# Kernel optimization log

Hardware: AMD Instinct MI355X
Metric: run time of the kernel (lower is better)

The kernel has to match this reference:

```python
import jax, jax.numpy as jnp
import numpy as np

SEQ = 4096
EMB = 2048
DQ = 2048
DV = 2048

def setup_inputs() -> dict:
    key = jax.random.key(0)
    k1, k2, k3, k4 = jax.random.split(key, 4)
    scale = 1.0 / np.sqrt(EMB)
    return {
        "embedding_word": jax.random.normal(k1, (SEQ, EMB), dtype=jnp.float32),
        "w_q": jax.random.normal(k2, (DQ, EMB), dtype=jnp.float32) * scale,
        "w_k": jax.random.normal(k3, (DQ, EMB), dtype=jnp.float32) * scale,
        "w_v": jax.random.normal(k4, (DV, EMB), dtype=jnp.float32) * scale,
    }

def reference(embedding_word, w_q, w_k, w_v):
    # nn.Linear: y = x @ W.T (bias=False)
    q = embedding_word @ w_q.T            # [S, d_q]
    k = embedding_word @ w_k.T            # [S, d_q]
    v = embedding_word @ w_v.T            # [S, d_v]
    scores = q @ k.T                      # [S, S]
    S = scores.shape[0]
    causal = jnp.tril(jnp.ones((S, S), dtype=bool))  # True = keep
    masked = jnp.where(causal, scores, -jnp.inf)
    weights = jax.nn.softmax(masked / jnp.sqrt(jnp.float32(DQ)), axis=-1)
    return weights @ v                    # [S, d_v]
```

## Files before the change

kernel.cpp:

```cpp
#include <hip/hip_runtime.h>


using u16 = unsigned short;
typedef __bf16 bf16x8 __attribute__((ext_vector_type(8)));
typedef float  f32x4  __attribute__((ext_vector_type(4)));
typedef u16    u16x8  __attribute__((ext_vector_type(8)));

__device__ __forceinline__ u16 f2b(float f) {
  union { float f; unsigned u; } x; x.f = f;
  unsigned r = x.u + 0x7fffu + ((x.u >> 16) & 1u);
  return (u16)(r >> 16);
}
__device__ __forceinline__ float b2f(u16 h) {
  union { unsigned u; float f; } x; x.u = ((unsigned)h) << 16;
  return x.f;
}

#define GLL16(src, dst)                                                        \
  __builtin_amdgcn_global_load_lds(                                            \
      (const __attribute__((address_space(1))) void*)(src),                    \
      (__attribute__((address_space(3))) void*)(dst), 16, 0, 0)

#define MFMA_BF16(a, b, c) __builtin_amdgcn_mfma_f32_16x16x32_bf16(a, b, c, 0, 0, 0)

__global__ __launch_bounds__(256)
void cast_all(const float* __restrict__ x, const float* __restrict__ wq,
              const float* __restrict__ wk, const float* __restrict__ wv,
              u16* __restrict__ dst) {
  const int b = blockIdx.x;
  const float* src;
  size_t off;
  if (b < 4096)      { src = x;  off = (size_t)b * 2048; }
  else if (b < 6144) { src = wq; off = (size_t)(b - 4096) * 2048; }
  else if (b < 8192) { src = wk; off = (size_t)(b - 6144) * 2048; }
  else               { src = wv; off = (size_t)(b - 8192) * 2048; }
  const size_t e = off + (size_t)threadIdx.x * 8;
  float4 a = *(const float4*)(src + e);
  float4 c = *(const float4*)(src + e + 4);
  u16x8 o;
  o[0] = f2b(a.x); o[1] = f2b(a.y); o[2] = f2b(a.z); o[3] = f2b(a.w);
  o[4] = f2b(c.x); o[5] = f2b(c.y); o[6] = f2b(c.z); o[7] = f2b(c.w);
  *(u16x8*)(dst + (size_t)b * 2048 + (size_t)threadIdx.x * 8) = o;
}

__global__ __launch_bounds__(512)
void gemm_qk256(const u16* __restrict__ A, const u16* __restrict__ W,
                u16* __restrict__ Qo, u16* __restrict__ Ko) {
  extern __shared__ char lds[];
  constexpr int NT = 32;
  const int bn = blockIdx.x, bm = blockIdx.y;
  const int tid = threadIdx.x;
  const int w = tid >> 6, lane = tid & 63;
  const int wr = w >> 2, wc = w & 3;
  const int l15 = lane & 15, l4 = lane >> 4;
  const int rs = lane >> 3;
  const int csw = ((lane & 7) ^ rs) << 3;
  const int m0 = bm * 256, n0 = bn * 256;

  const u16* gA = A + (size_t)(m0 + w * 8 + rs) * 2048 + csw;
  const u16* gB = W + (size_t)(n0 + w * 8 + rs) * 2048 + csw;
  char* lw = lds + w * 1024;
  const u16* sm = (const u16*)lds;

  auto stA = [&](int p, int u, int tt) {
    GLL16(gA + (size_t)(u * 64) * 2048 + tt * 64, lw + p * 65536 + u * 8192);
  };
  auto stB = [&](int p, int u, int tt) {
    GLL16(gB + (size_t)(u * 64) * 2048 + tt * 64,
          lw + p * 65536 + 32768 + u * 8192);
  };
  const int swz = (l15 & 7) << 3;
  auto rdA = [&](int p, int m, int kk) -> bf16x8 {
    int u = wr * 2 + (m >> 2);
    int r64 = (m & 3) * 16 + l15;
    int e = p * 32768 + u * 4096 + ((r64 * 64 + kk * 32 + l4 * 8) ^ swz);
    return *(const bf16x8*)&sm[e];
  };
  auto rdB = [&](int p, int n, int kk) -> bf16x8 {
    int e = p * 32768 + 16384 + wc * 4096 +
            (((n * 16 + l15) * 64 + kk * 32 + l4 * 8) ^ swz);
    return *(const bf16x8*)&sm[e];
  };

  f32x4 acc[8][4] = {};
  bf16x8 a0[4][2], a1[4][2], b0[2][2], b1[2][2];

  stA(0,0,0); stA(0,1,0); stA(0,2,0); stA(0,3,0);
  stB(0,0,0); stB(0,1,0); stB(0,2,0); stB(0,3,0);
  stA(1,0,1); stA(1,1,1); stA(1,2,1); stA(1,3,1);
  stB(1,0,1); stB(1,1,1); stB(1,2,1); stB(1,3,1);
  asm volatile("s_waitcnt vmcnt(8)" ::: "memory");
  __builtin_amdgcn_sched_barrier(0);
  __builtin_amdgcn_s_barrier();

  for (int t = 0; t < NT; ++t) {
    const int p = t & 1;
    const bool pre = (t + 2 < NT);
#pragma unroll
    for (int m = 0; m < 4; ++m) { a0[m][0] = rdA(p, m, 0); a0[m][1] = rdA(p, m, 1); }
#pragma unroll
    for (int n = 0; n < 2; ++n) { b0[n][0] = rdB(p, n, 0); b0[n][1] = rdB(p, n, 1); }
    __builtin_amdgcn_s_barrier();
    asm volatile("s_waitcnt lgkmcnt(0)" ::: "memory");
    __builtin_amdgcn_sched_barrier(0);
    __builtin_amdgcn_s_setprio(1);
#pragma unroll
    for (int m = 0; m < 4; ++m)
#pragma unroll
      for (int n = 0; n < 2; ++n)
#pragma unroll
        for (int kk = 0; kk < 2; ++kk)
          acc[m][n] = MFMA_BF16(a0[m][kk], b0[n][kk], acc[m][n]);
    __builtin_amdgcn_s_setprio(0);
    __builtin_amdgcn_s_barrier();
    if (pre) { stA(p, 0, t + 2); stA(p, 2, t + 2); }
#pragma unroll
    for (int n = 0; n < 2; ++n) { b1[n][0] = rdB(p, n + 2, 0); b1[n][1] = rdB(p, n + 2, 1); }
    __builtin_amdgcn_s_barrier();
    asm volatile("s_waitcnt lgkmcnt(0)" ::: "memory");
    __builtin_amdgcn_sched_barrier(0);
    __builtin_amdgcn_s_setprio(1);
#pragma unroll
    for (int m = 0; m < 4; ++m)
#pragma unroll
      for (int n = 0; n < 2; ++n)
#pragma unroll
        for (int kk = 0; kk < 2; ++kk)
          acc[m][n + 2] = MFMA_BF16(a0[m][kk], b1[n][kk], acc[m][n + 2]);
    __builtin_amdgcn_s_setprio(0);
    __builtin_amdgcn_s_barrier();
    if (pre) { stB(p, 0, t + 2); stB(p, 1, t + 2); }
#pragma unroll
    for (int m = 0; m < 4; ++m) { a1[m][0] = rdA(p, m + 4, 0); a1[m][1] = rdA(p, m + 4, 1); }
    __builtin_amdgcn_s_barrier();
    asm volatile("s_waitcnt lgkmcnt(0)" ::: "memory");
    __builtin_amdgcn_sched_barrier(0);
    __builtin_amdgcn_s_setprio(1);
#pragma unroll
    for (int m = 0; m < 4; ++m)
#pragma unroll
      for (int n = 0; n < 2; ++n)
#pragma unroll
        for (int kk = 0; kk < 2; ++kk)
          acc[m + 4][n] = MFMA_BF16(a1[m][kk], b0[n][kk], acc[m + 4][n]);
    __builtin_amdgcn_s_setprio(0);
    __builtin_amdgcn_s_barrier();
    if (pre) { stA(p, 1, t + 2); stA(p, 3, t + 2); stB(p, 2, t + 2); stB(p, 3, t + 2); }
    __builtin_amdgcn_s_setprio(1);
#pragma unroll
    for (int m = 0; m < 4; ++m)
#pragma unroll
      for (int n = 0; n < 2; ++n)
#pragma unroll
        for (int kk = 0; kk < 2; ++kk)
          acc[m + 4][n + 2] = MFMA_BF16(a1[m][kk], b1[n][kk], acc[m + 4][n + 2]);
    __builtin_amdgcn_s_setprio(0);
    if (pre)                { asm volatile("s_waitcnt vmcnt(8)" ::: "memory"); }
    else if (t + 1 < NT)    { asm volatile("s_waitcnt vmcnt(0)" ::: "memory"); }
    __builtin_amdgcn_sched_barrier(0);
    __builtin_amdgcn_s_barrier();
  }

  const int row0 = m0 + wr * 128 + l4 * 4;
  if (bn < 8) {
    const int cg0 = bn * 256 + wc * 64 + l15;
#pragma unroll
    for (int m = 0; m < 8; ++m)
#pragma unroll
      for (int n = 0; n < 4; ++n)
#pragma unroll
        for (int j = 0; j < 4; ++j)
          Qo[(size_t)(row0 + m * 16 + j) * 2048 + cg0 + n * 16] = f2b(acc[m][n][j]);
  } else {
    const int cg0 = bn * 256 - 2048 + wc * 64 + l15;
#pragma unroll
    for (int m = 0; m < 8; ++m)
#pragma unroll
      for (int n = 0; n < 4; ++n)
#pragma unroll
        for (int j = 0; j < 4; ++j)
          Ko[(size_t)(row0 + m * 16 + j) * 2048 + cg0 + n * 16] = f2b(acc[m][n][j]);
  }
}

__global__ __launch_bounds__(512)
void gemm_qkv(const u16* __restrict__ A, const u16* __restrict__ W,
              u16* __restrict__ Qo, u16* __restrict__ Ko,
              u16* __restrict__ VTo, int bn_base) {
  extern __shared__ char lds[];
  constexpr int NT = 32;
  const int bn = blockIdx.x + bn_base, bm = blockIdx.y;
  const int tid = threadIdx.x;
  const int w = tid >> 6, lane = tid & 63;
  const int wr = w >> 1, wc = w & 1;
  const int l15 = lane & 15, l4 = lane >> 4;
  const int rs = lane >> 3;
  const int csw = ((lane & 7) ^ rs) << 3;
  const int m0 = bm * 256, n0 = bn * 128;

  const u16* gA = A + (size_t)(m0 + w * 8 + rs) * 2048 + csw;
  const u16* gB = W + (size_t)(n0 + w * 8 + rs) * 2048 + csw;
  char* lw = lds + w * 1024;
  const u16* sm = (const u16*)lds;

  auto stA = [&](int p, int u, int tt) {
    GLL16(gA + (size_t)u * 64 * 2048 + tt * 64, lw + p * 49152 + u * 8192);
  };
  auto stB = [&](int p, int u, int tt) {
    GLL16(gB + (size_t)u * 64 * 2048 + tt * 64, lw + p * 49152 + 32768 + u * 8192);
  };
  const int swz = (l15 & 7) << 3;
  auto rdA = [&](int p, int m, int kk) -> bf16x8 {
    int e = p * 24576 + wr * 4096 + (((m * 16 + l15) * 64 + kk * 32 + l4 * 8) ^ swz);
    return *(const bf16x8*)&sm[e];
  };
  auto rdB = [&](int p, int n, int kk) -> bf16x8 {
    int e = p * 24576 + 16384 + wc * 4096 +
            (((n * 16 + l15) * 64 + kk * 32 + l4 * 8) ^ swz);
    return *(const bf16x8*)&sm[e];
  };

  f32x4 acc[4][4] = {};
  bf16x8 aE[4][2], aO[4][2], b01E[2][2], b01O[2][2], b23E[2][2], b23O[2][2];

  stA(0,0,0); stA(0,1,0); stA(0,2,0); stA(0,3,0); stB(0,0,0); stB(0,1,0);
  stA(1,0,1); stA(1,1,1); stA(1,2,1); stA(1,3,1); stB(1,0,1); stB(1,1,1);
  asm volatile("s_waitcnt vmcnt(6)" ::: "memory");
  __builtin_amdgcn_sched_barrier(0);
  __builtin_amdgcn_s_barrier();
#pragma unroll
  for (int m = 0; m < 4; ++m) { aE[m][0] = rdA(0,m,0); aE[m][1] = rdA(0,m,1); }
#pragma unroll
  for (int n = 0; n < 2; ++n) { b01E[n][0] = rdB(0,n,0); b01E[n][1] = rdB(0,n,1); }
  asm volatile("s_waitcnt lgkmcnt(0)" ::: "memory");
  __builtin_amdgcn_sched_barrier(0);
  __builtin_amdgcn_s_barrier();

  for (int i = 0; i < NT / 2; ++i) {
    const int te = 2 * i, to = 2 * i + 1;
    if (te + 2 < NT) { stA(0,0,te+2); stA(0,1,te+2); stA(0,2,te+2); }
#pragma unroll
    for (int n = 0; n < 2; ++n) { b23E[n][0] = rdB(0,n+2,0); b23E[n][1] = rdB(0,n+2,1); }
    __builtin_amdgcn_s_barrier();
    __builtin_amdgcn_s_setprio(1);
#pragma unroll
    for (int m = 0; m < 4; ++m)
#pragma unroll
      for (int n = 0; n < 2; ++n)
#pragma unroll
        for (int kk = 0; kk < 2; ++kk)
          acc[m][n] = MFMA_BF16(aE[m][kk], b01E[n][kk], acc[m][n]);
    __builtin_amdgcn_s_setprio(0);
    asm volatile("s_waitcnt lgkmcnt(0)" ::: "memory");
    __builtin_amdgcn_sched_barrier(0);
    __builtin_amdgcn_s_barrier();
    if (te + 2 < NT) {
      stA(0,3,te+2); stB(0,0,te+2); stB(0,1,te+2);
      asm volatile("s_waitcnt vmcnt(6)" ::: "memory");
    } else {
      asm volatile("s_waitcnt vmcnt(0)" ::: "memory");
    }
    __builtin_amdgcn_sched_barrier(0);
    __builtin_amdgcn_s_barrier();
#pragma unroll
    for (int m = 0; m < 4; ++m) { aO[m][0] = rdA(1,m,0); aO[m][1] = rdA(1,m,1); }
#pragma unroll
    for (int n = 0; n < 2; ++n) { b01O[n][0] = rdB(1,n,0); b01O[n][1] = rdB(1,n,1); }
    __builtin_amdgcn_s_setprio(1);
#pragma unroll
    for (int m = 0; m < 4; ++m)
#pragma unroll
      for (int n = 0; n < 2; ++n)
#pragma unroll
        for (int kk = 0; kk < 2; ++kk)
          acc[m][n+2] = MFMA_BF16(aE[m][kk], b23E[n][kk], acc[m][n+2]);
    __builtin_amdgcn_s_setprio(0);
    asm volatile("s_waitcnt lgkmcnt(0)" ::: "memory");
    __builtin_amdgcn_sched_barrier(0);
    __builtin_amdgcn_s_barrier();
    if (to + 2 < NT) { stA(1,0,to+2); stA(1,1,to+2); stA(1,2,to+2); }
#pragma unroll
    for (int n = 0; n < 2; ++n) { b23O[n][0] = rdB(1,n+2,0); b23O[n][1] = rdB(1,n+2,1); }
    __builtin_amdgcn_s_barrier();
    __builtin_amdgcn_s_setprio(1);
#pragma unroll
    for (int m = 0; m < 4; ++m)
#pragma unroll
      for (int n = 0; n < 2; ++n)
#pragma unroll
        for (int kk = 0; kk < 2; ++kk)
          acc[m][n] = MFMA_BF16(aO[m][kk], b01O[n][kk], acc[m][n]);
    __builtin_amdgcn_s_setprio(0);
    asm volatile("s_waitcnt lgkmcnt(0)" ::: "memory");
    __builtin_amdgcn_sched_barrier(0);
    __builtin_amdgcn_s_barrier();
    if (to + 2 < NT) {
      stA(1,3,to+2); stB(1,0,to+2); stB(1,1,to+2);
      asm volatile("s_waitcnt vmcnt(6)" ::: "memory");
    } else if (to + 1 < NT) {
      asm volatile("s_waitcnt vmcnt(0)" ::: "memory");
    }
    __builtin_amdgcn_sched_barrier(0);
    __builtin_amdgcn_s_barrier();
    if (to + 1 < NT) {
#pragma unroll
      for (int m = 0; m < 4; ++m) { aE[m][0] = rdA(0,m,0); aE[m][1] = rdA(0,m,1); }
#pragma unroll
      for (int n = 0; n < 2; ++n) { b01E[n][0] = rdB(0,n,0); b01E[n][1] = rdB(0,n,1); }
    }
    __builtin_amdgcn_s_setprio(1);
#pragma unroll
    for (int m = 0; m < 4; ++m)
#pragma unroll
      for (int n = 0; n < 2; ++n)
#pragma unroll
        for (int kk = 0; kk < 2; ++kk)
          acc[m][n+2] = MFMA_BF16(aO[m][kk], b23O[n][kk], acc[m][n+2]);
    __builtin_amdgcn_s_setprio(0);
    asm volatile("s_waitcnt lgkmcnt(0)" ::: "memory");
    __builtin_amdgcn_sched_barrier(0);
    __builtin_amdgcn_s_barrier();
  }

  const int row0 = m0 + wr * 64 + l4 * 4;
  const int cg0 = n0 + wc * 64 + l15;
  if (bn < 16) {
#pragma unroll
    for (int m = 0; m < 4; ++m)
#pragma unroll
      for (int n = 0; n < 4; ++n)
#pragma unroll
        for (int j = 0; j < 4; ++j)
          Qo[(size_t)(row0 + m * 16 + j) * 2048 + cg0 + n * 16] = f2b(acc[m][n][j]);
  } else if (bn < 32) {
#pragma unroll
    for (int m = 0; m < 4; ++m)
#pragma unroll
      for (int n = 0; n < 4; ++n)
#pragma unroll
        for (int j = 0; j < 4; ++j)
          Ko[(size_t)(row0 + m * 16 + j) * 2048 + (cg0 + n * 16 - 2048)] = f2b(acc[m][n][j]);
  } else {
#pragma unroll
    for (int m = 0; m < 4; ++m)
#pragma unroll
      for (int n = 0; n < 4; ++n)
#pragma unroll
        for (int j = 0; j < 4; ++j)
          VTo[(size_t)(cg0 + n * 16 - 4096) * 4096 + row0 + m * 16 + j] = f2b(acc[m][n][j]);
  }
}

template<int MODE>
__global__ __launch_bounds__(256)
void pipe128(const u16* __restrict__ A, const u16* __restrict__ B,
             void* __restrict__ C, float alpha) {
  extern __shared__ char lds[];
  constexpr int LDA = (MODE == 0) ? 2048 : 4096;
  constexpr int LDB = (MODE == 0) ? 2048 : 4096;

  int bm, bn, kt0 = 0;
  bool accum = false;
  if (MODE == 0) {
    const int b = blockIdx.x;
    int r = (int)((sqrtf(8.f * (float)b + 1.f) - 1.f) * 0.5f);
    while ((r + 1) * (r + 2) / 2 <= b) ++r;
    while (r * (r + 1) / 2 > b) --r;
    bm = r; bn = b - r * (r + 1) / 2;
  } else if (MODE == 1) {
    bm = 16 + (blockIdx.x >> 4); bn = blockIdx.x & 15;
  } else {
    const int g = blockIdx.x >> 4;
    bn = blockIdx.x & 15;
    if ((g & 1) == 0) { bm = 31 - (g >> 1); kt0 = 32; accum = true; }
    else              { bm = 15 - (g >> 1); }
  }
  const int NT = (MODE == 0 || MODE == 1) ? 32 : (2 * (bm + 1) - kt0);

  const int tid = threadIdx.x;
  const int w = tid >> 6, lane = tid & 63;
  const int wr = w >> 1, wc = w & 1;
  const int l15 = lane & 15, l4 = lane >> 4;
  const int rs = lane >> 3;
  const int csw = ((lane & 7) ^ rs) << 3;
  const int m0 = bm * 128, n0 = bn * 128;

  const u16* gA = A + (size_t)(m0 + w * 8 + rs) * LDA + csw + (size_t)kt0 * 64;
  const u16* gB = B + (size_t)(n0 + w * 8 + rs) * LDB + csw + (size_t)kt0 * 64;
  char* lw = lds + w * 1024;
  const u16* sm = (const u16*)lds;

  auto stA = [&](int p, int u, int tt) {
    GLL16(gA + (size_t)(u * 32) * LDA + tt * 64, lw + p * 32768 + u * 4096);
  };
  auto stB = [&](int p, int u, int tt) {
    GLL16(gB + (size_t)(u * 32) * LDB + tt * 64, lw + p * 32768 + 16384 + u * 4096);
  };
  const int swz = (l15 & 7) << 3;
  auto rdA = [&](int p, int m, int kk) -> bf16x8 {
    int e = p * 16384 + wr * 4096 + (((m * 16 + l15) * 64 + kk * 32 + l4 * 8) ^ swz);
    return *(const bf16x8*)&sm[e];
  };
  auto rdB = [&](int p, int n, int kk) -> bf16x8 {
    int e = p * 16384 + 8192 + wc * 4096 +
            (((n * 16 + l15) * 64 + kk * 32 + l4 * 8) ^ swz);
    return *(const bf16x8*)&sm[e];
  };

  f32x4 acc[4][4] = {};
  bf16x8 aE[4][2], aO[4][2], b01E[2][2], b01O[2][2], b23E[2][2], b23O[2][2];

  stA(0,0,0); stA(0,1,0); stA(0,2,0); stA(0,3,0);
  stB(0,0,0); stB(0,1,0); stB(0,2,0); stB(0,3,0);
  stA(1,0,1); stA(1,1,1); stA(1,2,1); stA(1,3,1);
  stB(1,0,1); stB(1,1,1); stB(1,2,1); stB(1,3,1);
  asm volatile("s_waitcnt vmcnt(8)" ::: "memory");
  __builtin_amdgcn_sched_barrier(0);
  __builtin_amdgcn_s_barrier();
#pragma unroll
  for (int m = 0; m < 4; ++m) { aE[m][0] = rdA(0,m,0); aE[m][1] = rdA(0,m,1); }
#pragma unroll
  for (int n = 0; n < 2; ++n) { b01E[n][0] = rdB(0,n,0); b01E[n][1] = rdB(0,n,1); }
  asm volatile("s_waitcnt lgkmcnt(0)" ::: "memory");
  __builtin_amdgcn_sched_barrier(0);
  __builtin_amdgcn_s_barrier();

  for (int i = 0; i < (NT >> 1); ++i) {
    const int te = 2 * i, to = 2 * i + 1;
    if (te + 2 < NT) { stA(0,0,te+2); stA(0,1,te+2); stA(0,2,te+2); stA(0,3,te+2); }
#pragma unroll
    for (int n = 0; n < 2; ++n) { b23E[n][0] = rdB(0,n+2,0); b23E[n][1] = rdB(0,n+2,1); }
    __builtin_amdgcn_s_barrier();
    __builtin_amdgcn_s_setprio(1);
#pragma unroll
    for (int m = 0; m < 4; ++m)
#pragma unroll
      for (int n = 0; n < 2; ++n)
#pragma unroll
        for (int kk = 0; kk < 2; ++kk)
          acc[m][n] = MFMA_BF16(aE[m][kk], b01E[n][kk], acc[m][n]);
    __builtin_amdgcn_s_setprio(0);
    asm volatile("s_waitcnt lgkmcnt(0)" ::: "memory");
    __builtin_amdgcn_sched_barrier(0);
    __builtin_amdgcn_s_barrier();
    if (te + 2 < NT) {
      stB(0,0,te+2); stB(0,1,te+2); stB(0,2,te+2); stB(0,3,te+2);
      asm volatile("s_waitcnt vmcnt(8)" ::: "memory");
    } else {
      asm volatile("s_waitcnt vmcnt(0)" ::: "memory");
    }
    __builtin_amdgcn_sched_barrier(0);
    __builtin_amdgcn_s_barrier();
#pragma unroll
    for (int m = 0; m < 4; ++m) { aO[m][0] = rdA(1,m,0); aO[m][1] = rdA(1,m,1); }
#pragma unroll
    for (int n = 0; n < 2; ++n) { b01O[n][0] = rdB(1,n,0); b01O[n][1] = rdB(1,n,1); }
    __builtin_amdgcn_s_setprio(1);
#pragma unroll
    for (int m = 0; m < 4; ++m)
#pragma unroll
      for (int n = 0; n < 2; ++n)
#pragma unroll
        for (int kk = 0; kk < 2; ++kk)
          acc[m][n+2] = MFMA_BF16(aE[m][kk], b23E[n][kk], acc[m][n+2]);
    __builtin_amdgcn_s_setprio(0);
    asm volatile("s_waitcnt lgkmcnt(0)" ::: "memory");
    __builtin_amdgcn_sched_barrier(0);
    __builtin_amdgcn_s_barrier();
    if (to + 2 < NT) { stA(1,0,to+2); stA(1,1,to+2); stA(1,2,to+2); stA(1,3,to+2); }
#pragma unroll
    for (int n = 0; n < 2; ++n) { b23O[n][0] = rdB(1,n+2,0); b23O[n][1] = rdB(1,n+2,1); }
    __builtin_amdgcn_s_barrier();
    __builtin_amdgcn_s_setprio(1);
#pragma unroll
    for (int m = 0; m < 4; ++m)
#pragma unroll
      for (int n = 0; n < 2; ++n)
#pragma unroll
        for (int kk = 0; kk < 2; ++kk)
          acc[m][n] = MFMA_BF16(aO[m][kk], b01O[n][kk], acc[m][n]);
    __builtin_amdgcn_s_setprio(0);
    asm volatile("s_waitcnt lgkmcnt(0)" ::: "memory");
    __builtin_amdgcn_sched_barrier(0);
    __builtin_amdgcn_s_barrier();
    if (to + 2 < NT) {
      stB(1,0,to+2); stB(1,1,to+2); stB(1,2,to+2); stB(1,3,to+2);
      asm volatile("s_waitcnt vmcnt(8)" ::: "memory");
    } else if (to + 1 < NT) {
      asm volatile("s_waitcnt vmcnt(0)" ::: "memory");
    }
    __builtin_amdgcn_sched_barrier(0);
    __builtin_amdgcn_s_barrier();
    if (to + 1 < NT) {
#pragma unroll
      for (int m = 0; m < 4; ++m) { aE[m][0] = rdA(0,m,0); aE[m][1] = rdA(0,m,1); }
#pragma unroll
      for (int n = 0; n < 2; ++n) { b01E[n][0] = rdB(0,n,0); b01E[n][1] = rdB(0,n,1); }
    }
    __builtin_amdgcn_s_setprio(1);
#pragma unroll
    for (int m = 0; m < 4; ++m)
#pragma unroll
      for (int n = 0; n < 2; ++n)
#pragma unroll
        for (int kk = 0; kk < 2; ++kk)
          acc[m][n+2] = MFMA_BF16(aO[m][kk], b23O[n][kk], acc[m][n+2]);
    __builtin_amdgcn_s_setprio(0);
    asm volatile("s_waitcnt lgkmcnt(0)" ::: "memory");
    __builtin_amdgcn_sched_barrier(0);
    __builtin_amdgcn_s_barrier();
  }

  const int row0 = m0 + wr * 64 + l4 * 4;
  const int col0 = n0 + wc * 64 + l15;
  if (MODE == 0) {
    u16* Co = (u16*)C;
#pragma unroll
    for (int m = 0; m < 4; ++m)
#pragma unroll
      for (int n = 0; n < 4; ++n)
#pragma unroll
        for (int j = 0; j < 4; ++j)
          Co[(size_t)(row0 + m * 16 + j) * 4096 + col0 + n * 16] =
              f2b(acc[m][n][j] * alpha);
  } else {
    float* Co = (float*)C;
    if (MODE == 2 && accum) {
#pragma unroll
      for (int m = 0; m < 4; ++m)
#pragma unroll
        for (int n = 0; n < 4; ++n)
#pragma unroll
          for (int j = 0; j < 4; ++j)
            Co[(size_t)(row0 + m * 16 + j) * 2048 + col0 + n * 16] += acc[m][n][j];
    } else {
#pragma unroll
      for (int m = 0; m < 4; ++m)
#pragma unroll
        for (int n = 0; n < 4; ++n)
#pragma unroll
          for (int j = 0; j < 4; ++j)
            Co[(size_t)(row0 + m * 16 + j) * 2048 + col0 + n * 16] = acc[m][n][j];
    }
  }
}

__global__ __launch_bounds__(256)
void softmax_causal(u16* __restrict__ S) {
  const int i = blockIdx.x;
  const int t = threadIdx.x;
  u16* row = S + (size_t)i * 4096;

  u16x8 r0 = *(const u16x8*)(row + t * 16);
  u16x8 r1 = *(const u16x8*)(row + t * 16 + 8);

  float v[16];
  float mx = -__builtin_inff();
#pragma unroll
  for (int c = 0; c < 16; ++c) {
    int j = t * 16 + c;
    float x = b2f(c < 8 ? r0[c] : r1[c - 8]);
    v[c] = (j <= i) ? x : -__builtin_inff();
    mx = fmaxf(mx, v[c]);
  }
#pragma unroll
  for (int off = 32; off >= 1; off >>= 1) mx = fmaxf(mx, __shfl_xor(mx, off));
  __shared__ float red[8];
  if ((t & 63) == 0) red[t >> 6] = mx;
  __syncthreads();
  mx = fmaxf(fmaxf(red[0], red[1]), fmaxf(red[2], red[3]));

  float s = 0.f;
#pragma unroll
  for (int c = 0; c < 16; ++c) {
    float e = exp2f((v[c] - mx) * 1.4426950408889634f);
    v[c] = e;
    s += e;
  }
#pragma unroll
  for (int off = 32; off >= 1; off >>= 1) s += __shfl_xor(s, off);
  if ((t & 63) == 0) red[4 + (t >> 6)] = s;
  __syncthreads();
  s = red[4] + red[5] + red[6] + red[7];
  float inv = 1.0f / s;

  u16x8 o0, o1;
#pragma unroll
  for (int c = 0; c < 8; ++c) {
    o0[c] = f2b(v[c] * inv);
    o1[c] = f2b(v[c + 8] * inv);
  }
  *(u16x8*)(row + t * 16) = o0;
  *(u16x8*)(row + t * 16 + 8) = o1;
}

extern "C" void kernel_launch(void* const* d_in, const int* in_sizes, int n_in,
                              void* d_out, int out_size, void* d_ws, size_t ws_size,
                              hipStream_t stream) {
  const float* x  = (const float*)d_in[0];
  const float* wq = (const float*)d_in[1];
  const float* wk = (const float*)d_in[2];
  const float* wv = (const float*)d_in[3];

  u16* x_bf  = (u16*)d_ws;
  u16* wq_bf = x_bf  + (size_t)4096 * 2048;
  u16* K_bf  = wq_bf + (size_t)3 * 2048 * 2048;
  u16* VT_bf = K_bf  + (size_t)4096 * 2048;
  u16* S_bf  = VT_bf + (size_t)2048 * 4096;
  u16* Q_bf  = (u16*)d_out;

  const float alpha = 0.022097086912079612f;

  cast_all<<<dim3(10240), 256, 0, stream>>>(x, wq, wk, wv, x_bf);

  gemm_qk256<<<dim3(16, 16), 512, 131072, stream>>>(x_bf, wq_bf, Q_bf, K_bf);
  pipe128<0><<<dim3(528), 256, 65536, stream>>>(Q_bf, K_bf, S_bf, alpha);
  gemm_qkv<<<dim3(16, 16), 512, 98304, stream>>>(x_bf, wq_bf, Q_bf, K_bf, VT_bf, 32);
  softmax_causal<<<dim3(4096), 256, 0, stream>>>(S_bf);
  pipe128<1><<<dim3(256), 256, 65536, stream>>>(S_bf, VT_bf, d_out, 1.0f);
  pipe128<2><<<dim3(512), 256, 65536, stream>>>(S_bf, VT_bf, d_out, 1.0f);
}
```

Baseline: 244.3 us.

## Retile Q/K projection GEMM to 256x128 tiles with BK=32 double buffering

Replaces the 256x256, BK=64 Q/K projection GEMM with a 256x128 tile and a BK=32 double-buffered LDS pipeline using 48KB shared memory. The grid doubles to 512 blocks, and the smaller LDS footprint plus launch bounds hint aim to allow multiple blocks per CU for better occupancy and latency hiding. The pipeline is restructured into even/odd stages that interleave register prefetch of the next fragments with MFMAs. Each block now reuses fewer operands per load, which raises global and LDS traffic per FLOP and adds more barriers per k-step.

```diff
diff --git a/kernel.cpp b/kernel.cpp
--- a/kernel.cpp
+++ b/kernel.cpp
@@ -43,138 +43,145 @@
   *(u16x8*)(dst + (size_t)b * 2048 + (size_t)threadIdx.x * 8) = o;
 }
 
-__global__ __launch_bounds__(512)
-void gemm_qk256(const u16* __restrict__ A, const u16* __restrict__ W,
-                u16* __restrict__ Qo, u16* __restrict__ Ko) {
+__global__ __launch_bounds__(512, 4)
+void gemm_qk_bk32(const u16* __restrict__ A, const u16* __restrict__ W,
+                  u16* __restrict__ Qo, u16* __restrict__ Ko) {
   extern __shared__ char lds[];
-  constexpr int NT = 32;
+  constexpr int NT = 64;
   const int bn = blockIdx.x, bm = blockIdx.y;
   const int tid = threadIdx.x;
   const int w = tid >> 6, lane = tid & 63;
-  const int wr = w >> 2, wc = w & 3;
+  const int wr = w >> 1, wc = w & 1;
   const int l15 = lane & 15, l4 = lane >> 4;
-  const int rs = lane >> 3;
-  const int csw = ((lane & 7) ^ rs) << 3;
-  const int m0 = bm * 256, n0 = bn * 256;
-
-  const u16* gA = A + (size_t)(m0 + w * 8 + rs) * 2048 + csw;
-  const u16* gB = W + (size_t)(n0 + w * 8 + rs) * 2048 + csw;
-  char* lw = lds + w * 1024;
+  const int rs = lane >> 2;
+  const int cs = ((lane & 3) ^ (rs & 3)) << 3;
+  const int m0 = bm * 256, n0 = bn * 128;
+
+  const u16* gA = A + (size_t)(m0 + w * 16 + rs) * 2048 + cs;
+  const u16* gB = W + (size_t)(n0 + w * 16 + rs) * 2048 + cs;
   const u16* sm = (const u16*)lds;
 
-  auto stA = [&](int p, int u, int tt) {
-    GLL16(gA + (size_t)(u * 64) * 2048 + tt * 64, lw + p * 65536 + u * 8192);
-  };
-  auto stB = [&](int p, int u, int tt) {
-    GLL16(gB + (size_t)(u * 64) * 2048 + tt * 64,
-          lw + p * 65536 + 32768 + u * 8192);
-  };
-  const int swz = (l15 & 7) << 3;
-  auto rdA = [&](int p, int m, int kk) -> bf16x8 {
-    int u = wr * 2 + (m >> 2);
-    int r64 = (m & 3) * 16 + l15;
-    int e = p * 32768 + u * 4096 + ((r64 * 64 + kk * 32 + l4 * 8) ^ swz);
-    return *(const bf16x8*)&sm[e];
-  };
-  auto rdB = [&](int p, int n, int kk) -> bf16x8 {
-    int e = p * 32768 + 16384 + wc * 4096 +
-            (((n * 16 + l15) * 64 + kk * 32 + l4 * 8) ^ swz);
-    return *(const bf16x8*)&sm[e];
-  };
-
-  f32x4 acc[8][4] = {};
-  bf16x8 a0[4][2], a1[4][2], b0[2][2], b1[2][2];
-
-  stA(0,0,0); stA(0,1,0); stA(0,2,0); stA(0,3,0);
-  stB(0,0,0); stB(0,1,0); stB(0,2,0); stB(0,3,0);
-  stA(1,0,1); stA(1,1,1); stA(1,2,1); stA(1,3,1);
-  stB(1,0,1); stB(1,1,1); stB(1,2,1); stB(1,3,1);
-  asm volatile("s_waitcnt vmcnt(8)" ::: "memory");
+  auto stA = [&](int p, int g, int tt) {
+    GLL16(gA + (size_t)(g * 128) * 2048 + tt * 32,
+          lds + p * 24576 + g * 8192 + w * 1024);
+  };
+  auto stB = [&](int p, int tt) {
+    GLL16(gB + tt * 32, lds + p * 24576 + 16384 + w * 1024);
+  };
+  const int swz = (l4 ^ (l15 & 3)) << 3;
+  auto rdA = [&](int p, int m) -> bf16x8 {
+    int row = wr * 64 + m * 16 + l15;
+    return *(const bf16x8*)&sm[p * 12288 + row * 32 + swz];
+  };
+  auto rdB = [&](int p, int n) -> bf16x8 {
+    int row = wc * 64 + n * 16 + l15;
+    return *(const bf16x8*)&sm[p * 12288 + 8192 + row * 32 + swz];
+  };
+
+  f32x4 acc[4][4] = {};
+  bf16x8 aE[4], aO[4], b01E[2], b01O[2], b23E[2], b23O[2];
+
+  stA(0, 0, 0); stA(0, 1, 0); stB(0, 0);
+  stA(1, 0, 1); stA(1, 1, 1); stB(1, 1);
+  asm volatile("s_waitcnt vmcnt(3)" ::: "memory");
   __builtin_amdgcn_sched_barrier(0);
   __builtin_amdgcn_s_barrier();
-
-  for (int t = 0; t < NT; ++t) {
-    const int p = t & 1;
-    const bool pre = (t + 2 < NT);
-#pragma unroll
-    for (int m = 0; m < 4; ++m) { a0[m][0] = rdA(p, m, 0); a0[m][1] = rdA(p, m, 1); }
-#pragma unroll
-    for (int n = 0; n < 2; ++n) { b0[n][0] = rdB(p, n, 0); b0[n][1] = rdB(p, n, 1); }
-    __builtin_amdgcn_s_barrier();
-    asm volatile("s_waitcnt lgkmcnt(0)" ::: "memory");
-    __builtin_amdgcn_sched_barrier(0);
-    __builtin_amdgcn_s_setprio(1);
-#pragma unroll
-    for (int m = 0; m < 4; ++m)
-#pragma unroll
-      for (int n = 0; n < 2; ++n)
-#pragma unroll
-        for (int kk = 0; kk < 2; ++kk)
-          acc[m][n] = MFMA_BF16(a0[m][kk], b0[n][kk], acc[m][n]);
-    __builtin_amdgcn_s_setprio(0);
-    __builtin_amdgcn_s_barrier();
-    if (pre) { stA(p, 0, t + 2); stA(p, 2, t + 2); }
-#pragma unroll
-    for (int n = 0; n < 2; ++n) { b1[n][0] = rdB(p, n + 2, 0); b1[n][1] = rdB(p, n + 2, 1); }
-    __builtin_amdgcn_s_barrier();
-    asm volatile("s_waitcnt lgkmcnt(0)" ::: "memory");
-    __builtin_amdgcn_sched_barrier(0);
-    __builtin_amdgcn_s_setprio(1);
-#pragma unroll
-    for (int m = 0; m < 4; ++m)
-#pragma unroll
-      for (int n = 0; n < 2; ++n)
-#pragma unroll
-        for (int kk = 0; kk < 2; ++kk)
-          acc[m][n + 2] = MFMA_BF16(a0[m][kk], b1[n][kk], acc[m][n + 2]);
-    __builtin_amdgcn_s_setprio(0);
-    __builtin_amdgcn_s_barrier();
-    if (pre) { stB(p, 0, t + 2); stB(p, 1, t + 2); }
-#pragma unroll
-    for (int m = 0; m < 4; ++m) { a1[m][0] = rdA(p, m + 4, 0); a1[m][1] = rdA(p, m + 4, 1); }
-    __builtin_amdgcn_s_barrier();
-    asm volatile("s_waitcnt lgkmcnt(0)" ::: "memory");
-    __builtin_amdgcn_sched_barrier(0);
-    __builtin_amdgcn_s_setprio(1);
-#pragma unroll
-    for (int m = 0; m < 4; ++m)
-#pragma unroll
-      for (int n = 0; n < 2; ++n)
-#pragma unroll
-        for (int kk = 0; kk < 2; ++kk)
-          acc[m + 4][n] = MFMA_BF16(a1[m][kk], b0[n][kk], acc[m + 4][n]);
-    __builtin_amdgcn_s_setprio(0);
-    __builtin_amdgcn_s_barrier();
-    if (pre) { stA(p, 1, t + 2); stA(p, 3, t + 2); stB(p, 2, t + 2); stB(p, 3, t + 2); }
-    __builtin_amdgcn_s_setprio(1);
-#pragma unroll
-    for (int m = 0; m < 4; ++m)
-#pragma unroll
-      for (int n = 0; n < 2; ++n)
-#pragma unroll
-        for (int kk = 0; kk < 2; ++kk)
-          acc[m + 4][n + 2] = MFMA_BF16(a1[m][kk], b1[n][kk], acc[m + 4][n + 2]);
-    __builtin_amdgcn_s_setprio(0);
-    if (pre)                { asm volatile("s_waitcnt vmcnt(8)" ::: "memory"); }
-    else if (t + 1 < NT)    { asm volatile("s_waitcnt vmcnt(0)" ::: "memory"); }
-    __builtin_amdgcn_sched_barrier(0);
-    __builtin_amdgcn_s_barrier();
-  }
-
-  const int row0 = m0 + wr * 128 + l4 * 4;
-  if (bn < 8) {
-    const int cg0 = bn * 256 + wc * 64 + l15;
-#pragma unroll
-    for (int m = 0; m < 8; ++m)
+#pragma unroll
+  for (int m = 0; m < 4; ++m) aE[m] = rdA(0, m);
+  b01E[0] = rdB(0, 0); b01E[1] = rdB(0, 1);
+  asm volatile("s_waitcnt lgkmcnt(0)" ::: "memory");
+  __builtin_amdgcn_sched_barrier(0);
+  __builtin_amdgcn_s_barrier();
+
+  for (int i = 0; i < NT / 2; ++i) {
+    const int te = 2 * i, to = 2 * i + 1;
+    if (te + 2 < NT) { stA(0, 0, te + 2); stA(0, 1, te + 2); }
+    b23E[0] = rdB(0, 2); b23E[1] = rdB(0, 3);
+    __builtin_amdgcn_s_barrier();
+    __builtin_amdgcn_s_setprio(1);
+#pragma unroll
+    for (int m = 0; m < 4; ++m)
+#pragma unroll
+      for (int n = 0; n < 2; ++n)
+        acc[m][n] = MFMA_BF16(aE[m], b01E[n], acc[m][n]);
+    __builtin_amdgcn_s_setprio(0);
+    asm volatile("s_waitcnt lgkmcnt(0)" ::: "memory");
+    __builtin_amdgcn_sched_barrier(0);
+    __builtin_amdgcn_s_barrier();
+    if (te + 2 < NT) {
+      stB(0, te + 2);
+      asm volatile("s_waitcnt vmcnt(3)" ::: "memory");
+    } else {
+      asm volatile("s_waitcnt vmcnt(0)" ::: "memory");
+    }
+    __builtin_amdgcn_sched_barrier(0);
+    __builtin_amdgcn_s_barrier();
+#pragma unroll
+    for (int m = 0; m < 4; ++m) aO[m] = rdA(1, m);
+    b01O[0] = rdB(1, 0); b01O[1] = rdB(1, 1);
+    __builtin_amdgcn_s_setprio(1);
+#pragma unroll
+    for (int m = 0; m < 4; ++m)
+#pragma unroll
+      for (int n = 0; n < 2; ++n)
+        acc[m][n + 2] = MFMA_BF16(aE[m], b23E[n], acc[m][n + 2]);
+    __builtin_amdgcn_s_setprio(0);
+    asm volatile("s_waitcnt lgkmcnt(0)" ::: "memory");
+    __builtin_amdgcn_sched_barrier(0);
+    __builtin_amdgcn_s_barrier();
+    if (to + 2 < NT) { stA(1, 0, to + 2); stA(1, 1, to + 2); }
+    b23O[0] = rdB(1, 2); b23O[1] = rdB(1, 3);
+    __builtin_amdgcn_s_barrier();
+    __builtin_amdgcn_s_setprio(1);
+#pragma unroll
+    for (int m = 0; m < 4; ++m)
+#pragma unroll
+      for (int n = 0; n < 2; ++n)
+        acc[m][n] = MFMA_BF16(aO[m], b01O[n], acc[m][n]);
+    __builtin_amdgcn_s_setprio(0);
+    asm volatile("s_waitcnt lgkmcnt(0)" ::: "memory");
+    __builtin_amdgcn_sched_barrier(0);
+    __builtin_amdgcn_s_barrier();
+    if (to + 2 < NT) {
+      stB(1, to + 2);
+      asm volatile("s_waitcnt vmcnt(3)" ::: "memory");
+    } else if (to + 1 < NT) {
+      asm volatile("s_waitcnt vmcnt(0)" ::: "memory");
+    }
+    __builtin_amdgcn_sched_barrier(0);
+    __builtin_amdgcn_s_barrier();
+    if (to + 1 < NT) {
+#pragma unroll
+      for (int m = 0; m < 4; ++m) aE[m] = rdA(0, m);
+      b01E[0] = rdB(0, 0); b01E[1] = rdB(0, 1);
+    }
+    __builtin_amdgcn_s_setprio(1);
+#pragma unroll
+    for (int m = 0; m < 4; ++m)
+#pragma unroll
+      for (int n = 0; n < 2; ++n)
+        acc[m][n + 2] = MFMA_BF16(aO[m], b23O[n], acc[m][n + 2]);
+    __builtin_amdgcn_s_setprio(0);
+    asm volatile("s_waitcnt lgkmcnt(0)" ::: "memory");
+    __builtin_amdgcn_sched_barrier(0);
+    __builtin_amdgcn_s_barrier();
+  }
+
+  const int row0 = m0 + wr * 64 + l4 * 4;
+  const int colg = wc * 64 + l15;
+  if (bn < 16) {
+    const int cg0 = bn * 128 + colg;
+#pragma unroll
+    for (int m = 0; m < 4; ++m)
 #pragma unroll
       for (int n = 0; n < 4; ++n)
 #pragma unroll
         for (int j = 0; j < 4; ++j)
           Qo[(size_t)(row0 + m * 16 + j) * 2048 + cg0 + n * 16] = f2b(acc[m][n][j]);
   } else {
-    const int cg0 = bn * 256 - 2048 + wc * 64 + l15;
-#pragma unroll
-    for (int m = 0; m < 8; ++m)
+    const int cg0 = bn * 128 - 2048 + colg;
+#pragma unroll
+    for (int m = 0; m < 4; ++m)
 #pragma unroll
       for (int n = 0; n < 4; ++n)
 #pragma unroll
@@ -613,7 +620,7 @@
 
   cast_all<<<dim3(10240), 256, 0, stream>>>(x, wq, wk, wv, x_bf);
 
-  gemm_qk256<<<dim3(16, 16), 512, 131072, stream>>>(x_bf, wq_bf, Q_bf, K_bf);
+  gemm_qk_bk32<<<dim3(32, 16), 512, 49152, stream>>>(x_bf, wq_bf, Q_bf, K_bf);
   pipe128<0><<<dim3(528), 256, 65536, stream>>>(Q_bf, K_bf, S_bf, alpha);
   gemm_qkv<<<dim3(16, 16), 512, 98304, stream>>>(x_bf, wq_bf, Q_bf, K_bf, VT_bf, 32);
   softmax_causal<<<dim3(4096), 256, 0, stream>>>(S_bf);
```

Result: slower. 261.4 us (+7.0%).

## Unroll QK projection GEMM by two and prefetch LDS fragments across phases

Applied to the files above, without the earlier changes.

The 256x256 QK projection GEMM main loop is unrolled over even/odd buffers, using precomputed LDS read pointers and incrementing global pointers. LDS fragment reads for the next MFMA phase are issued before the current phase, gated by partial lgkmcnt waits, and several intermediate barriers are dropped. The other GEMM gets the same pointer-increment addressing for its global-to-LDS loads. The goal is to cut address arithmetic and hide LDS latency behind MFMAs, at the cost of more registers and more delicate wait-count correctness.

```diff
diff --git a/kernel.cpp b/kernel.cpp
--- a/kernel.cpp
+++ b/kernel.cpp
@@ -59,49 +59,67 @@
 
   const u16* gA = A + (size_t)(m0 + w * 8 + rs) * 2048 + csw;
   const u16* gB = W + (size_t)(n0 + w * 8 + rs) * 2048 + csw;
-  char* lw = lds + w * 1024;
-  const u16* sm = (const u16*)lds;
-
-  auto stA = [&](int p, int u, int tt) {
-    GLL16(gA + (size_t)(u * 64) * 2048 + tt * 64, lw + p * 65536 + u * 8192);
+  const u16* gA0 = gA;
+  const u16* gA1 = gA + (size_t)64 * 2048;
+  const u16* gA2 = gA + (size_t)128 * 2048;
+  const u16* gA3 = gA + (size_t)192 * 2048;
+  const u16* gB0 = gB;
+  const u16* gB1 = gB + (size_t)64 * 2048;
+  const u16* gB2 = gB + (size_t)128 * 2048;
+  const u16* gB3 = gB + (size_t)192 * 2048;
+#define DSTA(P, U) (lds + (P) * 65536 + (U) * 8192 + w * 1024)
+#define DSTB(P, U) (lds + (P) * 65536 + 32768 + (U) * 8192 + w * 1024)
+
+  const u16* smp = (const u16*)lds;
+  const int swz = (l15 & 7) << 3;
+  const int aoff0 = wr * 2 * 4096 + ((l15 * 64 + l4 * 8) ^ swz);
+  const int aoff1 = wr * 2 * 4096 + ((l15 * 64 + 32 + l4 * 8) ^ swz);
+  const int boff0 = 16384 + wc * 4096 + ((l15 * 64 + l4 * 8) ^ swz);
+  const int boff1 = 16384 + wc * 4096 + ((l15 * 64 + 32 + l4 * 8) ^ swz);
+  const u16* pA0k0 = smp + aoff0;
+  const u16* pA0k1 = smp + aoff1;
+  const u16* pA1k0 = smp + 32768 + aoff0;
+  const u16* pA1k1 = smp + 32768 + aoff1;
+  const u16* pB0k0 = smp + boff0;
+  const u16* pB0k1 = smp + boff1;
+  const u16* pB1k0 = smp + 32768 + boff0;
+  const u16* pB1k1 = smp + 32768 + boff1;
+
+  auto rdA = [&](const u16* base, int m) -> bf16x8 {
+    return *(const bf16x8*)(base + (m & 3) * 1024 + (m >> 2) * 4096);
   };
-  auto stB = [&](int p, int u, int tt) {
-    GLL16(gB + (size_t)(u * 64) * 2048 + tt * 64,
-          lw + p * 65536 + 32768 + u * 8192);
-  };
-  const int swz = (l15 & 7) << 3;
-  auto rdA = [&](int p, int m, int kk) -> bf16x8 {
-    int u = wr * 2 + (m >> 2);
-    int r64 = (m & 3) * 16 + l15;
-    int e = p * 32768 + u * 4096 + ((r64 * 64 + kk * 32 + l4 * 8) ^ swz);
-    return *(const bf16x8*)&sm[e];
-  };
-  auto rdB = [&](int p, int n, int kk) -> bf16x8 {
-    int e = p * 32768 + 16384 + wc * 4096 +
-            (((n * 16 + l15) * 64 + kk * 32 + l4 * 8) ^ swz);
-    return *(const bf16x8*)&sm[e];
+  auto rdB = [&](const u16* base, int n) -> bf16x8 {
+    return *(const bf16x8*)(base + n * 1024);
   };
 
   f32x4 acc[8][4] = {};
   bf16x8 a0[4][2], a1[4][2], b0[2][2], b1[2][2];
 
-  stA(0,0,0); stA(0,1,0); stA(0,2,0); stA(0,3,0);
-  stB(0,0,0); stB(0,1,0); stB(0,2,0); stB(0,3,0);
-  stA(1,0,1); stA(1,1,1); stA(1,2,1); stA(1,3,1);
-  stB(1,0,1); stB(1,1,1); stB(1,2,1); stB(1,3,1);
+  GLL16(gA0, DSTA(0, 0)); GLL16(gA1, DSTA(0, 1));
+  GLL16(gA2, DSTA(0, 2)); GLL16(gA3, DSTA(0, 3));
+  GLL16(gB0, DSTB(0, 0)); GLL16(gB1, DSTB(0, 1));
+  GLL16(gB2, DSTB(0, 2)); GLL16(gB3, DSTB(0, 3));
+  GLL16(gA0 + 64, DSTA(1, 0)); GLL16(gA1 + 64, DSTA(1, 1));
+  GLL16(gA2 + 64, DSTA(1, 2)); GLL16(gA3 + 64, DSTA(1, 3));
+  GLL16(gB0 + 64, DSTB(1, 0)); GLL16(gB1 + 64, DSTB(1, 1));
+  GLL16(gB2 + 64, DSTB(1, 2)); GLL16(gB3 + 64, DSTB(1, 3));
+  gA0 += 128; gA1 += 128; gA2 += 128; gA3 += 128;
+  gB0 += 128; gB1 += 128; gB2 += 128; gB3 += 128;
   asm volatile("s_waitcnt vmcnt(8)" ::: "memory");
   __builtin_amdgcn_sched_barrier(0);
   __builtin_amdgcn_s_barrier();
-
-  for (int t = 0; t < NT; ++t) {
-    const int p = t & 1;
-    const bool pre = (t + 2 < NT);
-#pragma unroll
-    for (int m = 0; m < 4; ++m) { a0[m][0] = rdA(p, m, 0); a0[m][1] = rdA(p, m, 1); }
-#pragma unroll
-    for (int n = 0; n < 2; ++n) { b0[n][0] = rdB(p, n, 0); b0[n][1] = rdB(p, n, 1); }
-    __builtin_amdgcn_s_barrier();
-    asm volatile("s_waitcnt lgkmcnt(0)" ::: "memory");
+#pragma unroll
+  for (int m = 0; m < 4; ++m) { a0[m][0] = rdA(pA0k0, m); a0[m][1] = rdA(pA0k1, m); }
+#pragma unroll
+  for (int n = 0; n < 2; ++n) { b0[n][0] = rdB(pB0k0, n); b0[n][1] = rdB(pB0k1, n); }
+
+  for (int i = 0; i < NT / 2; ++i) {
+    const int te = 2 * i, to = 2 * i + 1;
+    const bool preE = (te + 2 < NT), preO = (to + 2 < NT);
+    b1[0][0] = rdB(pB0k0, 2); b1[0][1] = rdB(pB0k1, 2);
+    b1[1][0] = rdB(pB0k0, 3); b1[1][1] = rdB(pB0k1, 3);
+    a1[0][0] = rdA(pA0k0, 4); a1[0][1] = rdA(pA0k1, 4);
+    asm volatile("s_waitcnt lgkmcnt(6)" ::: "memory");
     __builtin_amdgcn_sched_barrier(0);
     __builtin_amdgcn_s_setprio(1);
 #pragma unroll
@@ -113,11 +131,11 @@
           acc[m][n] = MFMA_BF16(a0[m][kk], b0[n][kk], acc[m][n]);
     __builtin_amdgcn_s_setprio(0);
     __builtin_amdgcn_s_barrier();
-    if (pre) { stA(p, 0, t + 2); stA(p, 2, t + 2); }
-#pragma unroll
-    for (int n = 0; n < 2; ++n) { b1[n][0] = rdB(p, n + 2, 0); b1[n][1] = rdB(p, n + 2, 1); }
-    __builtin_amdgcn_s_barrier();
-    asm volatile("s_waitcnt lgkmcnt(0)" ::: "memory");
+    if (preE) { GLL16(gA0, DSTA(0, 0)); GLL16(gA2, DSTA(0, 2)); }
+    a1[1][0] = rdA(pA0k0, 5); a1[1][1] = rdA(pA0k1, 5);
+    a1[2][0] = rdA(pA0k0, 6); a1[2][1] = rdA(pA0k1, 6);
+    a1[3][0] = rdA(pA0k0, 7); a1[3][1] = rdA(pA0k1, 7);
+    asm volatile("s_waitcnt lgkmcnt(6)" ::: "memory");
     __builtin_amdgcn_sched_barrier(0);
     __builtin_amdgcn_s_setprio(1);
 #pragma unroll
@@ -129,10 +147,8 @@
           acc[m][n + 2] = MFMA_BF16(a0[m][kk], b1[n][kk], acc[m][n + 2]);
     __builtin_amdgcn_s_setprio(0);
     __builtin_amdgcn_s_barrier();
-    if (pre) { stB(p, 0, t + 2); stB(p, 1, t + 2); }
-#pragma unroll
-    for (int m = 0; m < 4; ++m) { a1[m][0] = rdA(p, m + 4, 0); a1[m][1] = rdA(p, m + 4, 1); }
-    __builtin_amdgcn_s_barrier();
+    if (preE) { GLL16(gB0, DSTB(0, 0)); GLL16(gB1, DSTB(0, 1));
+                GLL16(gB2, DSTB(0, 2)); GLL16(gB3, DSTB(0, 3)); }
     asm volatile("s_waitcnt lgkmcnt(0)" ::: "memory");
     __builtin_amdgcn_sched_barrier(0);
     __builtin_amdgcn_s_setprio(1);
@@ -145,7 +161,7 @@
           acc[m + 4][n] = MFMA_BF16(a1[m][kk], b0[n][kk], acc[m + 4][n]);
     __builtin_amdgcn_s_setprio(0);
     __builtin_amdgcn_s_barrier();
-    if (pre) { stA(p, 1, t + 2); stA(p, 3, t + 2); stB(p, 2, t + 2); stB(p, 3, t + 2); }
+    if (preE) { GLL16(gA1, DSTA(0, 1)); GLL16(gA3, DSTA(0, 3)); }
     __builtin_amdgcn_s_setprio(1);
 #pragma unroll
     for (int m = 0; m < 4; ++m)
@@ -155,11 +171,84 @@
         for (int kk = 0; kk < 2; ++kk)
           acc[m + 4][n + 2] = MFMA_BF16(a1[m][kk], b1[n][kk], acc[m + 4][n + 2]);
     __builtin_amdgcn_s_setprio(0);
-    if (pre)                { asm volatile("s_waitcnt vmcnt(8)" ::: "memory"); }
-    else if (t + 1 < NT)    { asm volatile("s_waitcnt vmcnt(0)" ::: "memory"); }
-    __builtin_amdgcn_sched_barrier(0);
-    __builtin_amdgcn_s_barrier();
-  }
+    if (preE) { asm volatile("s_waitcnt vmcnt(8)" ::: "memory"); }
+    else      { asm volatile("s_waitcnt vmcnt(0)" ::: "memory"); }
+    __builtin_amdgcn_sched_barrier(0);
+    __builtin_amdgcn_s_barrier();
+#pragma unroll
+    for (int m = 0; m < 4; ++m) { a0[m][0] = rdA(pA1k0, m); a0[m][1] = rdA(pA1k1, m); }
+#pragma unroll
+    for (int n = 0; n < 2; ++n) { b0[n][0] = rdB(pB1k0, n); b0[n][1] = rdB(pB1k1, n); }
+    b1[0][0] = rdB(pB1k0, 2); b1[0][1] = rdB(pB1k1, 2);
+    b1[1][0] = rdB(pB1k0, 3); b1[1][1] = rdB(pB1k1, 3);
+    a1[0][0] = rdA(pA1k0, 4); a1[0][1] = rdA(pA1k1, 4);
+    asm volatile("s_waitcnt lgkmcnt(6)" ::: "memory");
+    __builtin_amdgcn_sched_barrier(0);
+    __builtin_amdgcn_s_setprio(1);
+#pragma unroll
+    for (int m = 0; m < 4; ++m)
+#pragma unroll
+      for (int n = 0; n < 2; ++n)
+#pragma unroll
+        for (int kk = 0; kk < 2; ++kk)
+          acc[m][n] = MFMA_BF16(a0[m][kk], b0[n][kk], acc[m][n]);
+    __builtin_amdgcn_s_setprio(0);
+    __builtin_amdgcn_s_barrier();
+    if (preO) { GLL16(gA0 + 64, DSTA(1, 0)); GLL16(gA2 + 64, DSTA(1, 2)); }
+    a1[1][0] = rdA(pA1k0, 5); a1[1][1] = rdA(pA1k1, 5);
+    a1[2][0] = rdA(pA1k0, 6); a1[2][1] = rdA(pA1k1, 6);
+    a1[3][0] = rdA(pA1k0, 7); a1[3][1] = rdA(pA1k1, 7);
+    asm volatile("s_waitcnt lgkmcnt(6)" ::: "memory");
+    __builtin_amdgcn_sched_barrier(0);
+    __builtin_amdgcn_s_setprio(1);
+#pragma unroll
+    for (int m = 0; m < 4; ++m)
+#pragma unroll
+      for (int n = 0; n < 2; ++n)
+#pragma unroll
+        for (int kk = 0; kk < 2; ++kk)
+          acc[m][n + 2] = MFMA_BF16(a0[m][kk], b1[n][kk], acc[m][n + 2]);
+    __builtin_amdgcn_s_setprio(0);
+    __builtin_amdgcn_s_barrier();
+    if (preO) { GLL16(gB0 + 64, DSTB(1, 0)); GLL16(gB1 + 64, DSTB(1, 1));
+                GLL16(gB2 + 64, DSTB(1, 2)); GLL16(gB3 + 64, DSTB(1, 3)); }
+    asm volatile("s_waitcnt lgkmcnt(0)" ::: "memory");
+    __builtin_amdgcn_sched_barrier(0);
+    __builtin_amdgcn_s_setprio(1);
+#pragma unroll
+    for (int m = 0; m < 4; ++m)
+#pragma unroll
+      for (int n = 0; n < 2; ++n)
+#pragma unroll
+        for (int kk = 0; kk < 2; ++kk)
+          acc[m + 4][n] = MFMA_BF16(a1[m][kk], b0[n][kk], acc[m + 4][n]);
+    __builtin_amdgcn_s_setprio(0);
+    __builtin_amdgcn_s_barrier();
+    if (preO) { GLL16(gA1 + 64, DSTA(1, 1)); GLL16(gA3 + 64, DSTA(1, 3)); }
+    __builtin_amdgcn_s_setprio(1);
+#pragma unroll
+    for (int m = 0; m < 4; ++m)
+#pragma unroll
+      for (int n = 0; n < 2; ++n)
+#pragma unroll
+        for (int kk = 0; kk < 2; ++kk)
+          acc[m + 4][n + 2] = MFMA_BF16(a1[m][kk], b1[n][kk], acc[m + 4][n + 2]);
+    __builtin_amdgcn_s_setprio(0);
+    if (preO)             { asm volatile("s_waitcnt vmcnt(8)" ::: "memory"); }
+    else if (to + 1 < NT) { asm volatile("s_waitcnt vmcnt(0)" ::: "memory"); }
+    __builtin_amdgcn_sched_barrier(0);
+    __builtin_amdgcn_s_barrier();
+    if (to + 1 < NT) {
+#pragma unroll
+      for (int m = 0; m < 4; ++m) { a0[m][0] = rdA(pA0k0, m); a0[m][1] = rdA(pA0k1, m); }
+#pragma unroll
+      for (int n = 0; n < 2; ++n) { b0[n][0] = rdB(pB0k0, n); b0[n][1] = rdB(pB0k1, n); }
+    }
+    gA0 += 128; gA1 += 128; gA2 += 128; gA3 += 128;
+    gB0 += 128; gB1 += 128; gB2 += 128; gB3 += 128;
+  }
+#undef DSTA
+#undef DSTB
 
   const int row0 = m0 + wr * 128 + l4 * 4;
   if (bn < 8) {
@@ -387,15 +476,19 @@
 
   const u16* gA = A + (size_t)(m0 + w * 8 + rs) * LDA + csw + (size_t)kt0 * 64;
   const u16* gB = B + (size_t)(n0 + w * 8 + rs) * LDB + csw + (size_t)kt0 * 64;
+  const u16* gA0 = gA;
+  const u16* gA1 = gA + (size_t)32 * LDA;
+  const u16* gA2 = gA + (size_t)64 * LDA;
+  const u16* gA3 = gA + (size_t)96 * LDA;
+  const u16* gB0 = gB;
+  const u16* gB1 = gB + (size_t)32 * LDB;
+  const u16* gB2 = gB + (size_t)64 * LDB;
+  const u16* gB3 = gB + (size_t)96 * LDB;
   char* lw = lds + w * 1024;
   const u16* sm = (const u16*)lds;
-
-  auto stA = [&](int p, int u, int tt) {
-    GLL16(gA + (size_t)(u * 32) * LDA + tt * 64, lw + p * 32768 + u * 4096);
-  };
-  auto stB = [&](int p, int u, int tt) {
-    GLL16(gB + (size_t)(u * 32) * LDB + tt * 64, lw + p * 32768 + 16384 + u * 4096);
-  };
+#define PDSTA(P, U) (lw + (P) * 32768 + (U) * 4096)
+#define PDSTB(P, U) (lw + (P) * 32768 + 16384 + (U) * 4096)
+
   const int swz = (l15 & 7) << 3;
   auto rdA = [&](int p, int m, int kk) -> bf16x8 {
     int e = p * 16384 + wr * 4096 + (((m * 16 + l15) * 64 + kk * 32 + l4 * 8) ^ swz);
@@ -410,10 +503,16 @@
   f32x4 acc[4][4] = {};
   bf16x8 aE[4][2], aO[4][2], b01E[2][2], b01O[2][2], b23E[2][2], b23O[2][2];
 
-  stA(0,0,0); stA(0,1,0); stA(0,2,0); stA(0,3,0);
-  stB(0,0,0); stB(0,1,0); stB(0,2,0); stB(0,3,0);
-  stA(1,0,1); stA(1,1,1); stA(1,2,1); stA(1,3,1);
-  stB(1,0,1); stB(1,1,1); stB(1,2,1); stB(1,3,1);
+  GLL16(gA0, PDSTA(0,0)); GLL16(gA1, PDSTA(0,1));
+  GLL16(gA2, PDSTA(0,2)); GLL16(gA3, PDSTA(0,3));
+  GLL16(gB0, PDSTB(0,0)); GLL16(gB1, PDSTB(0,1));
+  GLL16(gB2, PDSTB(0,2)); GLL16(gB3, PDSTB(0,3));
+  GLL16(gA0 + 64, PDSTA(1,0)); GLL16(gA1 + 64, PDSTA(1,1));
+  GLL16(gA2 + 64, PDSTA(1,2)); GLL16(gA3 + 64, PDSTA(1,3));
+  GLL16(gB0 + 64, PDSTB(1,0)); GLL16(gB1 + 64, PDSTB(1,1));
+  GLL16(gB2 + 64, PDSTB(1,2)); GLL16(gB3 + 64, PDSTB(1,3));
+  gA0 += 128; gA1 += 128; gA2 += 128; gA3 += 128;
+  gB0 += 128; gB1 += 128; gB2 += 128; gB3 += 128;
   asm volatile("s_waitcnt vmcnt(8)" ::: "memory");
   __builtin_amdgcn_sched_barrier(0);
   __builtin_amdgcn_s_barrier();
@@ -427,7 +526,8 @@
 
   for (int i = 0; i < (NT >> 1); ++i) {
     const int te = 2 * i, to = 2 * i + 1;
-    if (te + 2 < NT) { stA(0,0,te+2); stA(0,1,te+2); stA(0,2,te+2); stA(0,3,te+2); }
+    if (te + 2 < NT) { GLL16(gA0, PDSTA(0,0)); GLL16(gA1, PDSTA(0,1));
+                       GLL16(gA2, PDSTA(0,2)); GLL16(gA3, PDSTA(0,3)); }
 #pragma unroll
     for (int n = 0; n < 2; ++n) { b23E[n][0] = rdB(0,n+2,0); b23E[n][1] = rdB(0,n+2,1); }
     __builtin_amdgcn_s_barrier();
@@ -444,7 +544,8 @@
     __builtin_amdgcn_sched_barrier(0);
     __builtin_amdgcn_s_barrier();
     if (te + 2 < NT) {
-      stB(0,0,te+2); stB(0,1,te+2); stB(0,2,te+2); stB(0,3,te+2);
+      GLL16(gB0, PDSTB(0,0)); GLL16(gB1, PDSTB(0,1));
+      GLL16(gB2, PDSTB(0,2)); GLL16(gB3, PDSTB(0,3));
       asm volatile("s_waitcnt vmcnt(8)" ::: "memory");
     } else {
       asm volatile("s_waitcnt vmcnt(0)" ::: "memory");
@@ -467,7 +568,8 @@
     asm volatile("s_waitcnt lgkmcnt(0)" ::: "memory");
     __builtin_amdgcn_sched_barrier(0);
     __builtin_amdgcn_s_barrier();
-    if (to + 2 < NT) { stA(1,0,to+2); stA(1,1,to+2); stA(1,2,to+2); stA(1,3,to+2); }
+    if (to + 2 < NT) { GLL16(gA0 + 64, PDSTA(1,0)); GLL16(gA1 + 64, PDSTA(1,1));
+                       GLL16(gA2 + 64, PDSTA(1,2)); GLL16(gA3 + 64, PDSTA(1,3)); }
 #pragma unroll
     for (int n = 0; n < 2; ++n) { b23O[n][0] = rdB(1,n+2,0); b23O[n][1] = rdB(1,n+2,1); }
     __builtin_amdgcn_s_barrier();
@@ -484,7 +586,8 @@
     __builtin_amdgcn_sched_barrier(0);
     __builtin_amdgcn_s_barrier();
     if (to + 2 < NT) {
-      stB(1,0,to+2); stB(1,1,to+2); stB(1,2,to+2); stB(1,3,to+2);
+      GLL16(gB0 + 64, PDSTB(1,0)); GLL16(gB1 + 64, PDSTB(1,1));
+      GLL16(gB2 + 64, PDSTB(1,2)); GLL16(gB3 + 64, PDSTB(1,3));
       asm volatile("s_waitcnt vmcnt(8)" ::: "memory");
     } else if (to + 1 < NT) {
       asm volatile("s_waitcnt vmcnt(0)" ::: "memory");
@@ -509,7 +612,11 @@
     asm volatile("s_waitcnt lgkmcnt(0)" ::: "memory");
     __builtin_amdgcn_sched_barrier(0);
     __builtin_amdgcn_s_barrier();
-  }
+    gA0 += 128; gA1 += 128; gA2 += 128; gA3 += 128;
+    gB0 += 128; gB1 += 128; gB2 += 128; gB3 += 128;
+  }
+#undef PDSTA
+#undef PDSTB
 
   const int row0 = m0 + wr * 64 + l4 * 4;
   const int col0 = n0 + wc * 64 + l15;
```

Result: slower. 250.1 us (+2.4%).
